# Kernel tuning notes

Hardware: AMD Instinct MI355X
Metric: run time of the kernel (lower is better)

Reference implementation:

```python
import jax, jax.numpy as jnp
import numpy as np

BN_EPS = 1e-5

def binary_activation(x):
    # ReActNet BinaryActivation: forward = sign(x), backward = piecewise poly STE
    out_fwd = jnp.sign(x)
    m1 = (x < -1.0).astype(x.dtype)
    m2 = (x < 0.0).astype(x.dtype)
    m3 = (x < 1.0).astype(x.dtype)
    out1 = -1.0 * m1 + (x * x + 2.0 * x) * (1.0 - m1)
    out2 = out1 * m2 + (-x * x + 2.0 * x) * (1.0 - m2)
    out3 = out2 * m3 + 1.0 * (1.0 - m3)
    return jax.lax.stop_gradient(out_fwd - out3) + out3

def binary_conv3x3(x, w, stride=1):
    # per-output-channel scaling = mean |w| over (in, kh, kw), detached
    scale = jax.lax.stop_gradient(jnp.mean(jnp.abs(w), axis=(1, 2, 3), keepdims=True))
    bw_no_grad = jax.lax.stop_gradient(scale * jnp.sign(w))
    cw = jnp.clip(w, -1.0, 1.0)
    bw = bw_no_grad - jax.lax.stop_gradient(cw) + cw
    return jax.lax.conv_general_dilated(
        x, bw, window_strides=(stride, stride), padding=[(1, 1), (1, 1)],
        dimension_numbers=('NCHW', 'OIHW', 'NCHW'))

def batchnorm_inference(y, gamma, beta, mean, var):
    inv = gamma * jax.lax.rsqrt(var + BN_EPS)
    return y * inv[None, :, None, None] + (beta - mean * inv)[None, :, None, None]

def setup_inputs() -> dict:
    key = jax.random.key(0)
    k1, k2, k3 = jax.random.split(key, 3)
    N, Cin, Cout, H, W = 64, 128, 128, 56, 56
    x = jax.random.normal(k1, (N, Cin, H, W), dtype=jnp.float32)
    weight = jax.random.normal(k2, (Cout, Cin, 3, 3), dtype=jnp.float32) * 0.1
    gamma = jnp.ones((Cout,), dtype=jnp.float32)
    beta = jnp.zeros((Cout,), dtype=jnp.float32)
    bn_mean = jnp.zeros((Cout,), dtype=jnp.float32)
    bn_var = jax.random.uniform(k3, (Cout,), dtype=jnp.float32)
    return {"x": x, "weight": weight, "gamma": gamma, "beta": beta,
            "bn_mean": bn_mean, "bn_var": bn_var}

def reference(x, weight, gamma, beta, bn_mean, bn_var):
    residual = x
    out = binary_activation(x)
    out = binary_conv3x3(out, weight, stride=1)
    out = batchnorm_inference(out, gamma, beta, bn_mean, bn_var)
    return out + residual
```

## Files before the change

### kernel.cpp

```cpp
#include <hip/hip_runtime.h>


#define N_   64
#define C_   128
#define H_   56
#define W_   56
#define HW_  (H_*W_)
#define PH_  (H_+2)
#define PW_  (W_+2)
#define PHW_ (PH_*PW_)
#define NPIX (N_*HW_)
#define NPAD (N_*PHW_)

typedef unsigned long long u64;

__global__ void prep_w_kernel(const float* __restrict__ w,
                              const float* __restrict__ gamma,
                              const float* __restrict__ beta,
                              const float* __restrict__ bn_mean,
                              const float* __restrict__ bn_var,
                              u64* __restrict__ wbits,
                              float* __restrict__ A, float* __restrict__ B) {
    const int o = blockIdx.x;
    const int lane = threadIdx.x;
    const float* wo = w + o * 1152;

    float s = 0.f;
    #pragma unroll
    for (int k = 0; k < 18; k++) s += fabsf(wo[k * 64 + lane]);
    #pragma unroll
    for (int off = 32; off > 0; off >>= 1) s += __shfl_down(s, off);
    float scale = __shfl(s, 0) * (1.0f / 1152.0f);

    #pragma unroll
    for (int t = 0; t < 9; t++) {
        #pragma unroll
        for (int j = 0; j < 2; j++) {
            float v = wo[(j * 64 + lane) * 9 + t];
            u64 b = __ballot(v < 0.0f);
            if (lane == 0) wbits[(o * 9 + t) * 2 + j] = b;
        }
    }
    if (lane == 0) {
        float inv = gamma[o] * rsqrtf(bn_var[o] + 1e-5f);
        A[o] = scale * inv;
        B[o] = beta[o] - bn_mean[o] * inv;
    }
}

__global__ void pack_x_kernel(const float* __restrict__ x,
                              ulonglong4* __restrict__ xb,
                              unsigned* __restrict__ xcnt) {
    int g = blockIdx.x * 256 + threadIdx.x;
    int n  = g / PHW_;
    int r  = g - n * PHW_;
    int ph = r / PW_;
    int pw = r - ph * PW_;
    int h = ph - 1, w = pw - 1;

    unsigned p0 = 0, p1 = 0, p2 = 0, p3 = 0;
    unsigned q0 = 0, q1 = 0, q2 = 0, q3 = 0;
    unsigned cnt = 0;

    if ((unsigned)h < (unsigned)H_ && (unsigned)w < (unsigned)W_) {
        const float* xp = x + (size_t)n * C_ * HW_ + h * W_ + w;
        #pragma unroll 16
        for (int c = 0; c < 32; c++) {
            float v = xp[(size_t)c * HW_];
            unsigned neg = (v < 0.f), nz = (v != 0.f);
            p0 |= neg << c; q0 |= nz << c; cnt += nz;
        }
        #pragma unroll 16
        for (int c = 0; c < 32; c++) {
            float v = xp[(size_t)(32 + c) * HW_];
            unsigned neg = (v < 0.f), nz = (v != 0.f);
            p1 |= neg << c; q1 |= nz << c; cnt += nz;
        }
        #pragma unroll 16
        for (int c = 0; c < 32; c++) {
            float v = xp[(size_t)(64 + c) * HW_];
            unsigned neg = (v < 0.f), nz = (v != 0.f);
            p2 |= neg << c; q2 |= nz << c; cnt += nz;
        }
        #pragma unroll 16
        for (int c = 0; c < 32; c++) {
            float v = xp[(size_t)(96 + c) * HW_];
            unsigned neg = (v < 0.f), nz = (v != 0.f);
            p3 |= neg << c; q3 |= nz << c; cnt += nz;
        }
    }
    ulonglong4 o4;
    o4.x = (u64)p0 | ((u64)p1 << 32);
    o4.y = (u64)p2 | ((u64)p3 << 32);
    o4.z = (u64)q0 | ((u64)q1 << 32);
    o4.w = (u64)q2 | ((u64)q3 << 32);
    xb[g]   = o4;
    xcnt[g] = cnt;
}

__global__ __launch_bounds__(256) void bconv_kernel(
        const ulonglong4* __restrict__ xb,
        const unsigned*   __restrict__ xcnt,
        const ulonglong2* __restrict__ wbits,
        const float* __restrict__ Ag, const float* __restrict__ Bg,
        const float* __restrict__ x, float* __restrict__ out) {
    __shared__ ulonglong2 w_s[1152];
    __shared__ float A_s[128], B_s[128];

    const int tid = threadIdx.x;
    for (int i = tid; i < 1152; i += 256) w_s[i] = wbits[i];
    if (tid < 128) { A_s[tid] = Ag[tid]; B_s[tid] = Bg[tid]; }
    __syncthreads();

    int g = blockIdx.x * 256 + tid;
    int n = g / HW_;
    int r = g - n * HW_;
    int h = r / W_;
    int w = r - h * W_;
    int pb = (n * PH_ + h + 1) * PW_ + (w + 1);

    u64 sx[9], sy[9], zx[9], zy[9];
    int cbase = 0;
    #pragma unroll
    for (int dh = 0; dh < 3; dh++) {
        #pragma unroll
        for (int dw = 0; dw < 3; dw++) {
            int idx = pb + (dh - 1) * PW_ + (dw - 1);
            int k = dh * 3 + dw;
            ulonglong4 t4 = xb[idx];
            sx[k] = t4.x; sy[k] = t4.y; zx[k] = t4.z; zy[k] = t4.w;
            cbase += (int)xcnt[idx];
        }
    }

    const float* xr = x   + (size_t)n * C_ * HW_ + r;
    float*       op = out + (size_t)n * C_ * HW_ + r;

    for (int o = 0; o < 128; o++) {
        int pc = 0;
        #pragma unroll
        for (int k = 0; k < 9; k++) {
            ulonglong2 ww = w_s[o * 9 + k];
            pc += __popcll((sx[k] ^ ww.x) & zx[k]);
            pc += __popcll((sy[k] ^ ww.y) & zy[k]);
        }
        float y = fmaf(A_s[o], (float)(cbase - 2 * pc), B_s[o]);
        op[(size_t)o * HW_] = y + xr[(size_t)o * HW_];
    }
}

extern "C" void kernel_launch(void* const* d_in, const int* in_sizes, int n_in,
                              void* d_out, int out_size, void* d_ws, size_t ws_size,
                              hipStream_t stream) {
    const float* x      = (const float*)d_in[0];
    const float* weight = (const float*)d_in[1];
    const float* gamma  = (const float*)d_in[2];
    const float* beta   = (const float*)d_in[3];
    const float* bnmean = (const float*)d_in[4];
    const float* bnvar  = (const float*)d_in[5];
    float* out = (float*)d_out;

    char* ws = (char*)d_ws;
    u64*        wbits = (u64*)ws;
    float*      A     = (float*)(ws + 18432);
    float*      B     = (float*)(ws + 18944);
    ulonglong4* xb    = (ulonglong4*)(ws + 19456);
    unsigned*   xcnt  = (unsigned*)(ws + 19456 + (size_t)NPAD * 32);

    prep_w_kernel<<<128, 64, 0, stream>>>(weight, gamma, beta, bnmean, bnvar,
                                          wbits, A, B);
    pack_x_kernel<<<NPAD / 256, 256, 0, stream>>>(x, xb, xcnt);
    bconv_kernel<<<NPIX / 256, 256, 0, stream>>>(xb, xcnt,
                                                 (const ulonglong2*)wbits, A, B,
                                                 x, out);
}
```

Baseline: 296.0 us.

## Add zero-free fast path with precomputed padding corrections and split output channels

```diff
diff --git a/kernel.cpp b/kernel.cpp
--- a/kernel.cpp
+++ b/kernel.cpp
@@ -48,9 +48,11 @@
     }
 }
 
-__global__ void pack_x_kernel(const float* __restrict__ x,
-                              ulonglong4* __restrict__ xb,
-                              unsigned* __restrict__ xcnt) {
+__global__ __launch_bounds__(256) void pack_x_kernel(
+        const float* __restrict__ x,
+        ulonglong2* __restrict__ xbs,
+        ulonglong2* __restrict__ xbz,
+        unsigned* __restrict__ xcnt) {
     int g = blockIdx.x * 256 + threadIdx.x;
     int n  = g / PHW_;
     int r  = g - n * PHW_;
@@ -58,58 +60,74 @@
     int pw = r - ph * PW_;
     int h = ph - 1, w = pw - 1;
 
-    unsigned p0 = 0, p1 = 0, p2 = 0, p3 = 0;
-    unsigned q0 = 0, q1 = 0, q2 = 0, q3 = 0;
-    unsigned cnt = 0;
+    unsigned p[4] = {0,0,0,0};
+    unsigned z[4] = {0,0,0,0};
 
     if ((unsigned)h < (unsigned)H_ && (unsigned)w < (unsigned)W_) {
-        const float* xp = x + (size_t)n * C_ * HW_ + h * W_ + w;
-        #pragma unroll 16
-        for (int c = 0; c < 32; c++) {
-            float v = xp[(size_t)c * HW_];
-            unsigned neg = (v < 0.f), nz = (v != 0.f);
-            p0 |= neg << c; q0 |= nz << c; cnt += nz;
-        }
-        #pragma unroll 16
-        for (int c = 0; c < 32; c++) {
-            float v = xp[(size_t)(32 + c) * HW_];
-            unsigned neg = (v < 0.f), nz = (v != 0.f);
-            p1 |= neg << c; q1 |= nz << c; cnt += nz;
-        }
-        #pragma unroll 16
-        for (int c = 0; c < 32; c++) {
-            float v = xp[(size_t)(64 + c) * HW_];
-            unsigned neg = (v < 0.f), nz = (v != 0.f);
-            p2 |= neg << c; q2 |= nz << c; cnt += nz;
-        }
-        #pragma unroll 16
-        for (int c = 0; c < 32; c++) {
-            float v = xp[(size_t)(96 + c) * HW_];
-            unsigned neg = (v < 0.f), nz = (v != 0.f);
-            p3 |= neg << c; q3 |= nz << c; cnt += nz;
-        }
-    }
-    ulonglong4 o4;
-    o4.x = (u64)p0 | ((u64)p1 << 32);
-    o4.y = (u64)p2 | ((u64)p3 << 32);
-    o4.z = (u64)q0 | ((u64)q1 << 32);
-    o4.w = (u64)q2 | ((u64)q3 << 32);
-    xb[g]   = o4;
-    xcnt[g] = cnt;
-}
-
-__global__ __launch_bounds__(256) void bconv_kernel(
-        const ulonglong4* __restrict__ xb,
+        const unsigned* xp =
+            (const unsigned*)(x + (size_t)n * C_ * HW_ + h * W_ + w);
+        #pragma unroll
+        for (int j = 0; j < 4; j++) {
+            unsigned pj = 0, zj = 0;
+            #pragma unroll
+            for (int c = 0; c < 32; c++) {
+                unsigned u = xp[(size_t)(j * 32 + c) * HW_];
+                pj |= (u >> 31) << c;
+                zj |= ((u << 1) != 0u ? 1u : 0u) << c;
+            }
+            p[j] = pj; z[j] = zj;
+        }
+    }
+    ulonglong2 s2, z2;
+    s2.x = (u64)p[0] | ((u64)p[1] << 32);
+    s2.y = (u64)p[2] | ((u64)p[3] << 32);
+    z2.x = (u64)z[0] | ((u64)z[1] << 32);
+    z2.y = (u64)z[2] | ((u64)z[3] << 32);
+    xbs[g] = s2;
+    xbz[g] = z2;
+    xcnt[g] = __popc(z[0]) + __popc(z[1]) + __popc(z[2]) + __popc(z[3]);
+}
+
+__device__ __forceinline__ int tapmask_of(int idx) {
+    int tm = 0;
+    if (idx & 1) tm |= 0x007;
+    if (idx & 2) tm |= 0x1C0;
+    if (idx & 4) tm |= 0x049;
+    if (idx & 8) tm |= 0x124;
+    return tm;
+}
+
+__global__ __launch_bounds__(256, 6) void bconv_kernel(
+        const ulonglong2* __restrict__ xbs,
+        const ulonglong2* __restrict__ xbz,
         const unsigned*   __restrict__ xcnt,
         const ulonglong2* __restrict__ wbits,
         const float* __restrict__ Ag, const float* __restrict__ Bg,
         const float* __restrict__ x, float* __restrict__ out) {
-    __shared__ ulonglong2 w_s[1152];
-    __shared__ float A_s[128], B_s[128];
+    __shared__ ulonglong2 w_s[576];
+    __shared__ int   psum_s[16 * 64];
+    __shared__ float A_s[64], B_s[64];
 
     const int tid = threadIdx.x;
-    for (int i = tid; i < 1152; i += 256) w_s[i] = wbits[i];
-    if (tid < 128) { A_s[tid] = Ag[tid]; B_s[tid] = Bg[tid]; }
+    const int obase = blockIdx.y * 64;
+
+    for (int i = tid; i < 576; i += 256) w_s[i] = wbits[obase * 9 + i];
+    if (tid < 64) { A_s[tid] = Ag[obase + tid]; B_s[tid] = Bg[obase + tid]; }
+    __syncthreads();
+
+    for (int e = tid; e < 1024; e += 256) {
+        int idx = e >> 6, o = e & 63;
+        int tm = tapmask_of(idx);
+        int s = 0;
+        #pragma unroll
+        for (int t = 0; t < 9; t++) {
+            if ((tm >> t) & 1) {
+                ulonglong2 ww = w_s[o * 9 + t];
+                s += 128 - 2 * (__popcll(ww.x) + __popcll(ww.y));
+            }
+        }
+        psum_s[e] = s;
+    }
     __syncthreads();
 
     int g = blockIdx.x * 256 + tid;
@@ -119,33 +137,57 @@
     int w = r - h * W_;
     int pb = (n * PH_ + h + 1) * PW_ + (w + 1);
 
-    u64 sx[9], sy[9], zx[9], zy[9];
-    int cbase = 0;
+    u64 sx[9], sy[9];
+    int taps_off[9];
+    int csum = 0;
     #pragma unroll
     for (int dh = 0; dh < 3; dh++) {
         #pragma unroll
         for (int dw = 0; dw < 3; dw++) {
+            int k = dh * 3 + dw;
             int idx = pb + (dh - 1) * PW_ + (dw - 1);
-            int k = dh * 3 + dw;
-            ulonglong4 t4 = xb[idx];
-            sx[k] = t4.x; sy[k] = t4.y; zx[k] = t4.z; zy[k] = t4.w;
-            cbase += (int)xcnt[idx];
-        }
-    }
-
-    const float* xr = x   + (size_t)n * C_ * HW_ + r;
-    float*       op = out + (size_t)n * C_ * HW_ + r;
-
-    for (int o = 0; o < 128; o++) {
-        int pc = 0;
-        #pragma unroll
-        for (int k = 0; k < 9; k++) {
-            ulonglong2 ww = w_s[o * 9 + k];
-            pc += __popcll((sx[k] ^ ww.x) & zx[k]);
-            pc += __popcll((sy[k] ^ ww.y) & zy[k]);
-        }
-        float y = fmaf(A_s[o], (float)(cbase - 2 * pc), B_s[o]);
-        op[(size_t)o * HW_] = y + xr[(size_t)o * HW_];
+            taps_off[k] = idx;
+            ulonglong2 t2 = xbs[idx];
+            sx[k] = t2.x; sy[k] = t2.y;
+            csum += (int)xcnt[idx];
+        }
+    }
+
+    int pidx = (h == 0 ? 1 : 0) | (h == H_-1 ? 2 : 0) |
+               (w == 0 ? 4 : 0) | (w == W_-1 ? 8 : 0);
+    int valid = 9 - __popc(tapmask_of(pidx));
+    bool slow = (csum != 128 * valid);
+
+    const float* xr = x   + ((size_t)n * C_ + obase) * HW_ + r;
+    float*       op = out + ((size_t)n * C_ + obase) * HW_ + r;
+    const int* psp = &psum_s[pidx * 64];
+
+    if (!slow) {
+        #pragma unroll 2
+        for (int o = 0; o < 64; o++) {
+            int pc = 0;
+            #pragma unroll
+            for (int k = 0; k < 9; k++) {
+                ulonglong2 ww = w_s[o * 9 + k];
+                pc += __popcll(sx[k] ^ ww.x);
+                pc += __popcll(sy[k] ^ ww.y);
+            }
+            int dot = 1152 - 2 * pc - psp[o];
+            op[o * HW_] = fmaf(A_s[o], (float)dot, B_s[o]) + xr[o * HW_];
+        }
+    } else {
+        for (int o = 0; o < 64; o++) {
+            int pc = 0;
+            #pragma unroll
+            for (int k = 0; k < 9; k++) {
+                ulonglong2 ww = w_s[o * 9 + k];
+                ulonglong2 zz = xbz[taps_off[k]];
+                pc += __popcll((sx[k] ^ ww.x) & zz.x);
+                pc += __popcll((sy[k] ^ ww.y) & zz.y);
+            }
+            int dot = csum - 2 * pc;
+            op[o * HW_] = fmaf(A_s[o], (float)dot, B_s[o]) + xr[o * HW_];
+        }
     }
 }
 
@@ -164,13 +206,15 @@
     u64*        wbits = (u64*)ws;
     float*      A     = (float*)(ws + 18432);
     float*      B     = (float*)(ws + 18944);
-    ulonglong4* xb    = (ulonglong4*)(ws + 19456);
+    ulonglong2* xbs   = (ulonglong2*)(ws + 19456);
+    ulonglong2* xbz   = (ulonglong2*)(ws + 19456 + (size_t)NPAD * 16);
     unsigned*   xcnt  = (unsigned*)(ws + 19456 + (size_t)NPAD * 32);
 
     prep_w_kernel<<<128, 64, 0, stream>>>(weight, gamma, beta, bnmean, bnvar,
                                           wbits, A, B);
-    pack_x_kernel<<<NPAD / 256, 256, 0, stream>>>(x, xb, xcnt);
-    bconv_kernel<<<NPIX / 256, 256, 0, stream>>>(xb, xcnt,
-                                                 (const ulonglong2*)wbits, A, B,
-                                                 x, out);
-}
+    pack_x_kernel<<<NPAD / 256, 256, 0, stream>>>(x, xbs, xbz, xcnt);
+    dim3 cgrid(NPIX / 256, 2);
+    bconv_kernel<<<cgrid, 256, 0, stream>>>(xbs, xbz, xcnt,
+                                            (const ulonglong2*)wbits, A, B,
+                                            x, out);
+}
```

After: 280.8 us. 5.1% less time.
